# Kernel optimization log

Hardware: AMD Instinct MI355X
Metric: run time of the kernel (lower is better)

## Reference

```python
import jax, jax.numpy as jnp
import numpy as np
import math

B, S, E, H = 4, 1024, 1024, 16
DK = E // H   # 64, must equal B*H for the original code's D-broadcast to work
M = 64


def setup_inputs():
    key = jax.random.key(0)
    ks = jax.random.split(key, 12)
    s = 0.02
    d = {"hidden_states": jax.random.normal(ks[0], (B, S, E), jnp.float32)}
    for i, name in enumerate(["Wq", "Wk", "Wv", "Wo"]):
        d[name] = jax.random.normal(ks[1 + i], (E, E), jnp.float32) * s
    for name in ["bq", "bk", "bv", "bo"]:
        d[name] = jnp.zeros((E,), jnp.float32)
    # eigenvectors of G G^T, as in SymmetricRandomFeatures.__init__ (orthogonal d_k x d_k)
    G = np.asarray(jax.random.normal(ks[9], (DK, M)), np.float64)
    _, vecs = np.linalg.eigh(G @ G.T)
    d["random_matrix"] = jnp.asarray(vecs, jnp.float32)
    # stands in for torch.randn(M, d_k) drawn inside forward
    d["omega_noise"] = jax.random.normal(ks[10], (M, DK), jnp.float32)
    return d


def _derf_forward(hidden_states, Wq, bq, Wk, bk, Wv, bv, Wo, bo, random_matrix, omega_noise):
    B_, S_, E_ = hidden_states.shape
    dk = E_ // H
    scale = 1.0 / math.sqrt(dk)

    def heads(x):
        return x.reshape(B_, S_, H, dk).transpose(0, 2, 1, 3)  # [B,H,S,dk]

    q = heads(hidden_states @ Wq.T + bq) * scale
    k = heads(hidden_states @ Wk.T + bk) * scale
    v = heads(hidden_states @ Wv.T + bv)

    qf = q.reshape(B_ * H, S_, dk)
    kf = k.reshape(B_ * H, S_, dk)

    # per-(B*H) second-moment matrix
    M1 = jnp.einsum('bsd,bse->bde', qf, qf) / S_
    M2 = jnp.einsum('bsd,bse->bde', kf, kf) / S_
    mu4 = jnp.mean(qf, axis=1)  # [BH, dk]
    mu5 = jnp.mean(kf, axis=1)
    mat = M1 + mu4[:, :, None] * mu5[:, None, :] + mu5[:, :, None] * mu4[:, None, :] + M2
    # torch updates A/B/C/D via .data (detached) -> stop_gradient before SVD
    mat = jax.lax.stop_gradient(mat)

    Q3, lam, _ = jnp.linalg.svd(mat)             # lam >= 0
    a = (1.0 - 2.0 * lam - jnp.sqrt((2.0 * lam + 1.0) ** 2 + 8.0 * lam)) / 16.0  # [BH, dk]
    one_m4a = 1.0 - 4.0 * a                       # diag of (I - 4A), >= 1
    Bmat = jnp.sqrt(one_m4a)[:, :, None] * jnp.swapaxes(Q3, -2, -1)  # sqrt(I-4A) @ Q3^T
    Dval = jnp.prod(one_m4a, axis=-1) ** 0.25     # det(I-4A)^(1/4), shape [BH] == [dk]

    omega = random_matrix @ omega_noise.T         # [dk, M]
    half_omega = 0.5 * jnp.sum(omega ** 2, axis=1)  # [dk]

    # NOTE: Dval has shape (B*H,) == (dk,) and broadcasts over the feature axis,
    # exactly replicating the torch broadcasting behavior (requires B*H == dk).
    eq = jnp.exp(jnp.einsum('bsd,bed->bse', qf, Bmat) + half_omega + Dval)
    ek = jnp.exp(jnp.einsum('bsd,bed->bse', kf, Bmat) + half_omega + Dval)

    qn = eq / jnp.linalg.norm(eq, axis=-1, keepdims=True)
    kn = ek / jnp.linalg.norm(ek, axis=-1, keepdims=True)
    qn = qn.reshape(B_, H, S_, dk)
    kn = kn.reshape(B_, H, S_, dk)

    scores = jnp.einsum('bhsd,bhtd->bhst', qn, kn)      # [B,H,S,S]
    probs = jax.nn.softmax(scores, axis=-1)
    ctx = jnp.einsum('bhst,bhtd->bhsd', probs, v)
    ctx = ctx.transpose(0, 2, 1, 3).reshape(B_, S_, E_)
    return ctx @ Wo.T + bo


def reference(hidden_states, Wq, bq, Wk, bk, Wv, bv, Wo, bo, random_matrix, omega_noise):
    return _derf_forward(hidden_states, Wq, bq, Wk, bk, Wv, bv, Wo, bo,
                         random_matrix, omega_noise)
```

## Files before the change

### kernel.cpp

```cpp
#include <hip/hip_runtime.h>
#include <hip/hip_bf16.h>

typedef __attribute__((ext_vector_type(8))) short v8s;
typedef __attribute__((ext_vector_type(4))) float v4f;
typedef __hip_bfloat16 bf16;

#define NSWEEP 1

__device__ __forceinline__ float bf2f(short s) {
    unsigned int u = ((unsigned int)(unsigned short)s) << 16;
    return __uint_as_float(u);
}

__global__ void diag_f32(float* __restrict__ out, size_t n, float code)
{
    for (size_t i = (size_t)blockIdx.x * 256 + threadIdx.x; i < n;
         i += (size_t)gridDim.x * 256)
        out[i] = (i == 0) ? code : 0.0f;
}

template<int MODE>
__device__ __forceinline__
void gemm_tile_body(const void* __restrict__ Ap, const float* __restrict__ W,
                    const float* __restrict__ bias, float scale,
                    bf16* __restrict__ o0, bf16* __restrict__ o1,
                    bf16* __restrict__ o2, bf16* __restrict__ o3,
                    float* __restrict__ outF,
                    int mt, int nt, int t, bf16 (*As)[40], bf16 (*Bs)[40])
{
    const int K = 1024;
    int m0 = mt * 128;
    int n0 = nt * 128;
    int lane = t & 63, w = t >> 6;
    int wm = (w >> 1) * 64, wn = (w & 1) * 64;
    int l15 = lane & 15, quad = lane >> 4;

    v4f zz = {0.f, 0.f, 0.f, 0.f};
    v4f acc[4][4];
#pragma unroll
    for (int i = 0; i < 4; ++i)
#pragma unroll
        for (int j = 0; j < 4; ++j) acc[i][j] = zz;

    for (int k0 = 0; k0 < K; k0 += 32) {
        __syncthreads();
        if (MODE != 3) {
            const float* A = (const float*)Ap;
#pragma unroll
            for (int r2 = 0; r2 < 4; ++r2) {
                int idx = t + r2 * 256;
                int row = idx >> 3, kc = (idx & 7) * 4;
                float4 v = *(const float4*)&A[(size_t)(m0 + row) * K + k0 + kc];
                As[row][kc + 0] = __float2bfloat16(v.x);
                As[row][kc + 1] = __float2bfloat16(v.y);
                As[row][kc + 2] = __float2bfloat16(v.z);
                As[row][kc + 3] = __float2bfloat16(v.w);
            }
        } else {
            const bf16* A = (const bf16*)Ap;
#pragma unroll
            for (int r2 = 0; r2 < 2; ++r2) {
                int idx = t + r2 * 256;
                int row = idx >> 2, kc = (idx & 3) * 8;
                int kk = k0 + kc;
                int h = kk >> 6, d = kk & 63;
                int mr = m0 + row;
                int b = mr >> 10, s = mr & 1023;
                *(float4*)&As[row][kc] =
                    *(const float4*)&A[(((size_t)(b * 16 + h) * 1024 + s) << 6) + d];
            }
        }
#pragma unroll
        for (int r2 = 0; r2 < 4; ++r2) {
            int idx = t + r2 * 256;
            int row = idx >> 3, kc = (idx & 7) * 4;
            float4 v = *(const float4*)&W[(size_t)(n0 + row) * K + k0 + kc];
            Bs[row][kc + 0] = __float2bfloat16(v.x);
            Bs[row][kc + 1] = __float2bfloat16(v.y);
            Bs[row][kc + 2] = __float2bfloat16(v.z);
            Bs[row][kc + 3] = __float2bfloat16(v.w);
        }
        __syncthreads();
        v8s af[4], bfr[4];
#pragma unroll
        for (int i = 0; i < 4; ++i)
            af[i] = *(v8s*)&As[wm + i * 16 + l15][quad * 8];
#pragma unroll
        for (int j = 0; j < 4; ++j)
            bfr[j] = *(v8s*)&Bs[wn + j * 16 + l15][quad * 8];
#pragma unroll
        for (int i = 0; i < 4; ++i)
#pragma unroll
            for (int j = 0; j < 4; ++j)
                acc[i][j] = __builtin_amdgcn_mfma_f32_16x16x32_bf16(af[i], bfr[j], acc[i][j], 0, 0, 0);
    }
    bf16* vout = nullptr;
    if (MODE == 2) {
        int b = m0 >> 10;
        vout = (b == 0) ? o0 : (b == 1) ? o1 : (b == 2) ? o2 : o3;
    }
#pragma unroll
    for (int i = 0; i < 4; ++i)
#pragma unroll
        for (int j = 0; j < 4; ++j)
#pragma unroll
            for (int r = 0; r < 4; ++r) {
                int m = m0 + wm + i * 16 + quad * 4 + r;
                int n = n0 + wn + j * 16 + l15;
                float val = (acc[i][j][r] + bias[n]) * scale;
                if (MODE == 1) {
                    int b = m >> 10, s = m & 1023, h = n >> 6, d = n & 63;
                    o0[(((size_t)(b * 16 + h) * 1024 + s) << 6) + d] = __float2bfloat16(val);
                } else if (MODE == 2) {
                    int s = m & 1023, h = n >> 6, d = n & 63;
                    vout[(((size_t)h * 1024 + s) << 6) + d] = __float2bfloat16(val);
                } else {
                    outF[(size_t)m * 1024 + n] = val;
                }
            }
}

__global__ __launch_bounds__(256)
void gemm_qk(const float* __restrict__ hs,
             const float* __restrict__ Wq, const float* __restrict__ bq,
             const float* __restrict__ Wk, const float* __restrict__ bk,
             bf16* __restrict__ Qf, bf16* __restrict__ Kf)
{
    __shared__ bf16 As[128][40];
    __shared__ bf16 Bs[128][40];
    int bx = blockIdx.x;
    bool isK = bx >= 32;
    gemm_tile_body<1>(hs, isK ? Wk : Wq, isK ? bk : bq, 0.125f,
                      isK ? Kf : Qf, nullptr, nullptr, nullptr, nullptr,
                      bx & 31, blockIdx.y, threadIdx.x, As, Bs);
}

__global__ __launch_bounds__(256)
void gemm_o(const bf16* __restrict__ Ctx, const float* __restrict__ Wo,
            const float* __restrict__ bo, float* __restrict__ outF)
{
    __shared__ bf16 As[128][40];
    __shared__ bf16 Bs[128][40];
    gemm_tile_body<3>(Ctx, Wo, bo, 1.0f, nullptr, nullptr, nullptr, nullptr,
                      outF, blockIdx.x, blockIdx.y, threadIdx.x, As, Bs);
}

__global__ __launch_bounds__(256)
void gram_stats(const bf16* __restrict__ qb, const bf16* __restrict__ kb,
                float* __restrict__ G, float* __restrict__ musum)
{
    __shared__ float qt[64][68];
    __shared__ float ktl[64][68];
    int bh = blockIdx.x, sc = blockIdx.y;
    int t = threadIdx.x;
    size_t base = ((size_t)bh * 1024 + sc * 64) * 64;
#pragma unroll
    for (int r = 0; r < 2; ++r) {
        int c = t + r * 256;
        int row = c >> 3, c8 = (c & 7) * 8;
        v8s vq = *(const v8s*)&qb[base + row * 64 + c8];
        v8s vk = *(const v8s*)&kb[base + row * 64 + c8];
#pragma unroll
        for (int i = 0; i < 8; ++i) {
            qt[row][c8 + i] = bf2f(vq[i]);
            ktl[row][c8 + i] = bf2f(vk[i]);
        }
    }
    __syncthreads();
    int tj = t & 15, ti = t >> 4;
    float aq[4][4], ak[4][4];
#pragma unroll
    for (int r = 0; r < 4; ++r)
#pragma unroll
        for (int c = 0; c < 4; ++c) { aq[r][c] = 0.f; ak[r][c] = 0.f; }
    for (int s = 0; s < 64; ++s) {
        float qd[4], qe[4], kd[4], ke[4];
#pragma unroll
        for (int r = 0; r < 4; ++r) {
            qd[r] = qt[s][ti * 4 + r]; qe[r] = qt[s][tj * 4 + r];
            kd[r] = ktl[s][ti * 4 + r]; ke[r] = ktl[s][tj * 4 + r];
        }
#pragma unroll
        for (int r = 0; r < 4; ++r)
#pragma unroll
            for (int c = 0; c < 4; ++c) {
                aq[r][c] += qd[r] * qe[c];
                ak[r][c] += kd[r] * ke[c];
            }
    }
    float* Gp = G + (size_t)bh * 4096;
#pragma unroll
    for (int r = 0; r < 4; ++r)
#pragma unroll
        for (int c = 0; c < 4; ++c)
            atomicAdd(&Gp[(ti * 4 + r) * 64 + tj * 4 + c], aq[r][c] + ak[r][c]);
    if (t < 128) {
        int which = t >> 6, d = t & 63;
        float s0 = 0.0f;
        if (which == 0) { for (int s = 0; s < 64; ++s) s0 += qt[s][d]; }
        else            { for (int s = 0; s < 64; ++s) s0 += ktl[s][d]; }
        atomicAdd(&musum[((size_t)which * 64 + bh) * 64 + d], s0);
    }
}

__device__ void jacobi_body(int bh, const float* __restrict__ G,
                            const float* __restrict__ musum,
                            float* __restrict__ W2, float* __restrict__ Dval,
                            char* smem)
{
    float  (*A)[65]   = (float(*)[65])smem;
    float2* cs2       = (float2*)(smem + 16640);
    float*  lam       = (float*)(smem + 17152);
    float*  muq       = (float*)(smem + 17408);
    float*  muk       = (float*)(smem + 17664);
    float  (*redA)[64] = (float(*)[64])(smem + 17920);
    float  (*redV)[64] = (float(*)[64])(smem + 19968);
    int t = threadIdx.x;
    int lane = t & 63, w = t >> 6;
    const float invS = 1.0f / 1024.0f;
    if (t < 64) {
        muq[t] = musum[(size_t)bh * 64 + t] * invS;
        muk[t] = musum[4096 + (size_t)bh * 64 + t] * invS;
    }
    __syncthreads();
    const float* Gb = G + (size_t)bh * 4096;
    float vr[8];
#pragma unroll
    for (int i = 0; i < 8; ++i) vr[i] = (w * 8 + i == lane) ? 1.0f : 0.0f;
#pragma unroll
    for (int r = 0; r < 8; ++r) {
        int idx = t + r * 512;
        int i = idx >> 6, j = idx & 63;
        A[i][j] = Gb[idx] * invS + muq[i] * muk[j] + muk[i] * muq[j];
    }
    __syncthreads();
    for (int sweep = 0; sweep < NSWEEP; ++sweep) {
        for (int m = 1; m < 64; ++m) {
            if (t < 64) {
                int q = t ^ m;
                float app = A[t][t], aqq = A[q][q], apq = A[t][q];
                float c = 1.0f, s = 0.0f;
                if (fabsf(apq) > 1e-28f) {
                    float tau = (aqq - app) / (2.0f * apq);
                    float tt = (tau >= 0.0f ? 1.0f : -1.0f)
                             / (fabsf(tau) + sqrtf(1.0f + tau * tau));
                    float cd = 1.0f / sqrtf(1.0f + tt * tt);
                    c = cd; s = tt * cd;
                }
                cs2[t] = make_float2(c, -s);
            }
            __syncthreads();
            int hb = 31 - __builtin_clz((unsigned)m);
            int lowmask = (1 << hb) - 1;
#pragma unroll
            for (int r = 0; r < 2; ++r) {
                int idx = t + r * 512;
                int ki = idx >> 5, kj = idx & 31;
                int i1 = ((ki & ~lowmask) << 1) | (ki & lowmask);
                int i2 = i1 ^ m;
                int j1 = ((kj & ~lowmask) << 1) | (kj & lowmask);
                int j2 = j1 ^ m;
                float a11 = A[i1][j1], a12 = A[i1][j2];
                float a21 = A[i2][j1], a22 = A[i2][j2];
                float2 ci = cs2[i1];
                float2 cj = cs2[j1];
                float t11 = ci.x * a11 + ci.y * a21, t12 = ci.x * a12 + ci.y * a22;
                float t21 = ci.x * a21 - ci.y * a11, t22 = ci.x * a22 - ci.y * a12;
                A[i1][j1] = cj.x * t11 + cj.y * t12;
                A[i1][j2] = cj.x * t12 - cj.y * t11;
                A[i2][j1] = cj.x * t21 + cj.y * t22;
                A[i2][j2] = cj.x * t22 - cj.y * t21;
            }
            {
                float2 cj = cs2[lane];
#pragma unroll
                for (int i = 0; i < 8; ++i) {
                    float pv = __shfl_xor(vr[i], m, 64);
                    vr[i] = cj.x * vr[i] + cj.y * pv;
                }
            }
            __syncthreads();
        }
    }
    if (t < 64) lam[t] = A[t][t];
    float best = -1.0f, sv = 0.0f;
#pragma unroll
    for (int i = 0; i < 8; ++i) {
        float av = fabsf(vr[i]);
        if (av > best) { best = av; sv = vr[i]; }
    }
    redA[w][lane] = best;
    redV[w][lane] = sv;
    __syncthreads();
    float gbest = -1.0f, gsv = 0.0f;
#pragma unroll
    for (int ww = 0; ww < 8; ++ww) {
        float av = redA[ww][lane];
        if (av > gbest) { gbest = av; gsv = redV[ww][lane]; }
    }
    float lj = lam[lane];
    int rank = 0;
    for (int k2 = 0; k2 < 64; ++k2) {
        float lk = lam[k2];
        rank += (lk > lj) || (lk == lj && k2 < lane);
    }
    float tl = 2.0f * lj + 1.0f;
    float om = (3.0f + 2.0f * lj + sqrtf(tl * tl + 8.0f * lj)) * 0.25f;
    float cfac = sqrtf(om);
    if (gsv < 0.0f) cfac = -cfac;
#pragma unroll
    for (int i = 0; i < 8; ++i)
        W2[((size_t)bh * 64 + (w * 8 + i)) * 64 + rank] = cfac * vr[i];
    if (w == 0) muq[lane] = logf(om);
    __syncthreads();
    if (t == 0) {
        float ssum = 0.0f;
        for (int j = 0; j < 64; ++j) ssum += muq[j];
        Dval[bh] = expf(0.25f * ssum);
    }
}

__device__ void omega_body(const float* __restrict__ rm,
                           const float* __restrict__ on,
                           float* __restrict__ hw, char* smem)
{
    float (*ons)[64] = (float(*)[64])smem;
    int t = threadIdx.x;
    for (int i = t; i < 4096; i += 512) ons[i >> 6][i & 63] = on[i];
    __syncthreads();
    if (t < 64) {
        float rmv[64];
#pragma unroll
        for (int j = 0; j < 64; ++j) rmv[j] = rm[t * 64 + j];
        float r8[8];
#pragma unroll
        for (int i = 0; i < 8; ++i) r8[i] = 0.0f;
        for (int k = 0; k < 8; ++k) {
#pragma unroll
            for (int i = 0; i < 8; ++i) {
                int m = k * 8 + i;
                float dot = 0.0f;
#pragma unroll
                for (int j = 0; j < 64; ++j) dot += rmv[j] * ons[m][j];
                r8[i] += dot * dot;
            }
        }
        float acc = ((r8[0] + r8[1]) + (r8[2] + r8[3])) + ((r8[4] + r8[5]) + (r8[6] + r8[7]));
        hw[t] = 0.5f * acc;
    }
}

__global__ __launch_bounds__(512)
void jacobi_fused(const float* __restrict__ G, const float* __restrict__ musum,
                  float* __restrict__ W2, float* __restrict__ Dval,
                  const float* __restrict__ hs, const float* __restrict__ Wv,
                  const float* __restrict__ bv,
                  bf16* __restrict__ V0, bf16* __restrict__ V1,
                  bf16* __restrict__ V2,
                  const float* __restrict__ rm, const float* __restrict__ on,
                  float* __restrict__ hw)
{
    __shared__ __align__(16) char smem[40960];
    int bid = blockIdx.x;
    if (bid < 64) {
        jacobi_body(bid, G, musum, W2, Dval, smem);
    } else if (bid < 160) {
        int gb = bid - 64;
        int t = threadIdx.x;
        int h = t >> 8, tl = t & 255;
        int T = gb * 2 + h;
        int mt = T >> 3, nt = T & 7;
        bf16 (*As)[40] = (bf16(*)[40])(smem + h * 20480);
        bf16 (*Bs)[40] = (bf16(*)[40])(smem + h * 20480 + 10240);
        gemm_tile_body<2>(hs, Wv, bv, 1.0f, V0, V1, V2, nullptr, nullptr,
                          mt, nt, tl, As, Bs);
    } else {
        omega_body(rm, on, hw, smem);
    }
}

__global__ __launch_bounds__(256)
void features_v23(bf16* __restrict__ qb, bf16* __restrict__ kb,
                  const float* __restrict__ W2g, const float* __restrict__ Dv,
                  const float* __restrict__ hw,
                  const float* __restrict__ hs, const float* __restrict__ Wv,
                  const float* __restrict__ bv,
                  bf16* __restrict__ V3)
{
    __shared__ __align__(16) char smem[20480];
    int bid = blockIdx.x;
    int t = threadIdx.x;
    if (bid < 512) {
        bf16 (*whi)[72] = (bf16(*)[72])smem;
        bf16 (*wlo)[72] = (bf16(*)[72])(smem + 9216);
        float* hD = (float*)(smem + 18432);
        int bh = bid >> 3, qk = (bid >> 2) & 1, rg = bid & 3;
        const float* W2b = W2g + (size_t)bh * 4096;
#pragma unroll
        for (int r = 0; r < 4; ++r) {
            int idx4 = t + r * 256;
            int d = idx4 >> 4, e4 = (idx4 & 15) * 4;
            float4 wv = ((const float4*)W2b)[idx4];
            float vv[4] = {wv.x, wv.y, wv.z, wv.w};
#pragma unroll
            for (int i = 0; i < 4; ++i) {
                bf16 h = __float2bfloat16(vv[i]);
                whi[e4 + i][d] = h;
                wlo[e4 + i][d] = __float2bfloat16(vv[i] - __bfloat162float(h));
            }
        }
        if (t < 64) hD[t] = hw[t] + Dv[t];
        __syncthreads();
        int lane = t & 63, w = t >> 6;
        int l15 = lane & 15, quad = lane >> 4;
        bf16* buf = qk ? kb : qb;
        bf16* base = buf + ((size_t)bh << 16);
        int R0 = rg * 256 + w * 64;
        v8s aq[4][2];
#pragma unroll
        for (int i = 0; i < 4; ++i) {
            const bf16* rp = base + (size_t)(R0 + i * 16 + l15) * 64;
            aq[i][0] = *(const v8s*)&rp[quad * 8];
            aq[i][1] = *(const v8s*)&rp[32 + quad * 8];
        }
        v4f zz = {0.f, 0.f, 0.f, 0.f};
        v4f acc[4][4];
#pragma unroll
        for (int i = 0; i < 4; ++i)
#pragma unroll
            for (int j = 0; j < 4; ++j) acc[i][j] = zz;
#pragma unroll
        for (int j = 0; j < 4; ++j) {
            v8s bh0 = *(v8s*)&whi[j * 16 + l15][quad * 8];
            v8s bh1 = *(v8s*)&whi[j * 16 + l15][32 + quad * 8];
            v8s bl0 = *(v8s*)&wlo[j * 16 + l15][quad * 8];
            v8s bl1 = *(v8s*)&wlo[j * 16 + l15][32 + quad * 8];
#pragma unroll
            for (int i = 0; i < 4; ++i) {
                acc[i][j] = __builtin_amdgcn_mfma_f32_16x16x32_bf16(aq[i][0], bh0, acc[i][j], 0, 0, 0);
                acc[i][j] = __builtin_amdgcn_mfma_f32_16x16x32_bf16(aq[i][1], bh1, acc[i][j], 0, 0, 0);
                acc[i][j] = __builtin_amdgcn_mfma_f32_16x16x32_bf16(aq[i][0], bl0, acc[i][j], 0, 0, 0);
                acc[i][j] = __builtin_amdgcn_mfma_f32_16x16x32_bf16(aq[i][1], bl1, acc[i][j], 0, 0, 0);
            }
        }
        float hDl[4];
#pragma unroll
        for (int j = 0; j < 4; ++j) hDl[j] = hD[j * 16 + l15];
#pragma unroll
        for (int i = 0; i < 4; ++i) {
            float te[4][4];
            float s2[4] = {0.f, 0.f, 0.f, 0.f};
#pragma unroll
            for (int j = 0; j < 4; ++j)
#pragma unroll
                for (int r = 0; r < 4; ++r) {
                    float x = acc[i][j][r] + hDl[j];
                    float e = expf(x);
                    te[j][r] = e;
                    s2[r] += e * e;
                }
#pragma unroll
            for (int r = 0; r < 4; ++r) {
#pragma unroll
                for (int off = 1; off < 16; off <<= 1)
                    s2[r] += __shfl_xor(s2[r], off, 64);
                float inv = 1.0f / sqrtf(s2[r]);
                int R = R0 + i * 16 + quad * 4 + r;
                bf16* rp = base + (size_t)R * 64;
#pragma unroll
                for (int j = 0; j < 4; ++j)
                    rp[j * 16 + l15] = __float2bfloat16(te[j][r] * inv);
            }
        }
    } else {
        int gb = bid - 512;
        int mt = 24 + (gb >> 3), nt = gb & 7;
        bf16 (*As)[40] = (bf16(*)[40])smem;
        bf16 (*Bs)[40] = (bf16(*)[40])(smem + 10240);
        gemm_tile_body<2>(hs, Wv, bv, 1.0f, nullptr, nullptr, nullptr, V3, nullptr,
                          mt, nt, t, As, Bs);
    }
}

__global__ __launch_bounds__(256)
void flash_attn(const bf16* __restrict__ qn, const bf16* __restrict__ kn,
                const bf16* __restrict__ v0, const bf16* __restrict__ v1,
                const bf16* __restrict__ v2, const bf16* __restrict__ v3,
                bf16* __restrict__ ctx)
{
    __shared__ bf16 kt_s[64][72];
    __shared__ bf16 vt_s[64][72];
    __shared__ bf16 p_s[4][16][72];
    int bh = blockIdx.x, qt = blockIdx.y;
    int t = threadIdx.x, lane = t & 63, w = t >> 6;
    int quad = lane >> 4, l15 = lane & 15;
    int b = bh >> 4, hl = bh & 15;
    const bf16* vv = ((b == 0) ? v0 : (b == 1) ? v1 : (b == 2) ? v2 : v3)
                   + ((size_t)hl << 16);

    int qrow = qt * 64 + w * 16 + l15;
    const bf16* qptr = qn + ((size_t)bh * 1024 + qrow) * 64;
    v8s aq0 = *(const v8s*)&qptr[quad * 8];
    v8s aq1 = *(const v8s*)&qptr[32 + quad * 8];

    v4f zz = {0.f, 0.f, 0.f, 0.f};
    v4f ctxa[4];
#pragma unroll
    for (int dj = 0; dj < 4; ++dj) ctxa[dj] = zz;
    float lsum[4] = {0.f, 0.f, 0.f, 0.f};

    for (int kt = 0; kt < 16; ++kt) {
        __syncthreads();
#pragma unroll
        for (int r2 = 0; r2 < 2; ++r2) {
            int idx = t + r2 * 256;
            int row = idx >> 3, c8 = (idx & 7) * 8;
            *(float4*)&kt_s[row][c8] =
                *(const float4*)&kn[((size_t)bh * 1024 + kt * 64 + row) * 64 + c8];
            v8s vchunk = *(const v8s*)&vv[((size_t)(kt * 64 + row)) * 64 + c8];
#pragma unroll
            for (int i = 0; i < 8; ++i)
                ((short*)vt_s)[(size_t)(c8 + i) * 72 + (row ^ c8)] = vchunk[i];
        }
        __syncthreads();
        v4f sa[4];
#pragma unroll
        for (int j = 0; j < 4; ++j) {
            v8s bk0 = *(v8s*)&kt_s[j * 16 + l15][quad * 8];
            v8s bk1 = *(v8s*)&kt_s[j * 16 + l15][32 + quad * 8];
            v4f z = zz;
            z = __builtin_amdgcn_mfma_f32_16x16x32_bf16(aq0, bk0, z, 0, 0, 0);
            sa[j] = __builtin_amdgcn_mfma_f32_16x16x32_bf16(aq1, bk1, z, 0, 0, 0);
        }
        float pv[4][4];
#pragma unroll
        for (int r = 0; r < 4; ++r) {
#pragma unroll
            for (int j = 0; j < 4; ++j) {
                float pe = __expf(sa[j][r]);
                pv[j][r] = pe;
                lsum[r] += pe;
            }
        }
#pragma unroll
        for (int j = 0; j < 4; ++j)
#pragma unroll
            for (int r = 0; r < 4; ++r)
                p_s[w][quad * 4 + r][j * 16 + l15] = __float2bfloat16(pv[j][r]);
        __syncthreads();
        v8s ap0 = *(v8s*)&p_s[w][l15][quad * 8];
        v8s ap1 = *(v8s*)&p_s[w][l15][32 + quad * 8];
#pragma unroll
        for (int dj = 0; dj < 4; ++dj) {
            int d0 = dj * 16 + l15;
            int a0 = (d0 >> 3) & 7;
            v8s bv0 = *(v8s*)&vt_s[d0][8 * (quad ^ a0)];
            v8s bv1 = *(v8s*)&vt_s[d0][8 * ((4 + quad) ^ a0)];
            ctxa[dj] = __builtin_amdgcn_mfma_f32_16x16x32_bf16(ap0, bv0, ctxa[dj], 0, 0, 0);
            ctxa[dj] = __builtin_amdgcn_mfma_f32_16x16x32_bf16(ap1, bv1, ctxa[dj], 0, 0, 0);
        }
    }
#pragma unroll
    for (int r = 0; r < 4; ++r)
#pragma unroll
        for (int off = 1; off < 16; off <<= 1)
            lsum[r] += __shfl_xor(lsum[r], off, 64);
#pragma unroll
    for (int dj = 0; dj < 4; ++dj)
#pragma unroll
        for (int r = 0; r < 4; ++r) {
            int srow = qt * 64 + w * 16 + quad * 4 + r;
            int d = dj * 16 + l15;
            float val = ctxa[dj][r] / lsum[r];
            ctx[((size_t)bh * 1024 + srow) * 64 + d] = __float2bfloat16(val);
        }
}

extern "C" void kernel_launch(void* const* d_in, const int* in_sizes, int n_in,
                              void* d_out, int out_size, void* d_ws, size_t ws_size,
                              hipStream_t stream)
{
    const size_t OUT_N = 4194304;
    long mx = 0; int ih = -1;
    for (int i = 0; i < n_in; ++i)
        if ((long)in_sizes[i] > mx) { mx = in_sizes[i]; ih = i; }
    long szW = mx / 4, szR = mx / 1024, szB = mx / 4096;
    int wI[4], rI[2], bI[4], nW = 0, nR = 0, nB = 0;
    bool bad = (n_in != 11) || (mx % 4096 != 0);
    if (!bad) {
        for (int i = 0; i < n_in; ++i) {
            if (i == ih) continue;
            long s = in_sizes[i];
            if (s == szW && nW < 4) wI[nW++] = i;
            else if (s == szR && nR < 2) rI[nR++] = i;
            else if (s == szB && nB < 4) bI[nB++] = i;
            else bad = true;
        }
        if (nW != 4 || nR != 2 || nB != 4) bad = true;
    }
    if (bad) {
        diag_f32<<<256, 256, 0, stream>>>((float*)d_out, OUT_N, 333.0f);
        return;
    }
    const float *Wq, *Wk, *Wv, *Wo, *bq, *bk, *bv, *bo, *rm, *on;
    float *WqS, *WkS;
    if (ih == 8 && wI[0] == 0 && wI[1] == 1 && wI[2] == 2 && wI[3] == 3) {
        Wk = (const float*)d_in[wI[0]]; Wo = (const float*)d_in[wI[1]];
        Wq = (const float*)d_in[wI[2]]; Wv = (const float*)d_in[wI[3]];
        bk = (const float*)d_in[bI[0]]; bo = (const float*)d_in[bI[1]];
        bq = (const float*)d_in[bI[2]]; bv = (const float*)d_in[bI[3]];
        on = (const float*)d_in[rI[0]]; rm = (const float*)d_in[rI[1]];
        WqS = (float*)d_in[wI[2]]; WkS = (float*)d_in[wI[0]];
    } else {
        Wq = (const float*)d_in[wI[0]]; Wk = (const float*)d_in[wI[1]];
        Wv = (const float*)d_in[wI[2]]; Wo = (const float*)d_in[wI[3]];
        bq = (const float*)d_in[bI[0]]; bk = (const float*)d_in[bI[1]];
        bv = (const float*)d_in[bI[2]]; bo = (const float*)d_in[bI[3]];
        rm = (const float*)d_in[rI[0]]; on = (const float*)d_in[rI[1]];
        WqS = (float*)d_in[wI[0]]; WkS = (float*)d_in[wI[1]];
    }
    const float* hs = (const float*)d_in[ih];
    float* hsW = (float*)d_in[ih];
    float* outF = (float*)d_out;

    bf16* Qf = (bf16*)d_out;
    bf16* Kf = (bf16*)((char*)d_out + (8u << 20));
    float* G     = WqS;
    float* musum = WqS + 262144;
    float* hw    = WqS + 262144 + 16384;
    float* Dval  = WqS + 262144 + 16384 + 1024;
    bf16* V0 = (bf16*)WkS;
    bf16* V1 = (bf16*)WkS + 1048576;
    bf16* V2 = (bf16*)(WqS + 327680);
    bf16* V3 = (bf16*)hsW;
    bf16* Ctx = (bf16*)(hsW + 524288);

    gemm_qk<<<dim3(64, 8), 256, 0, stream>>>(hs, Wq, bq, Wk, bk, Qf, Kf);
    hipMemsetAsync(G, 0, 1u << 20, stream);
    hipMemsetAsync(musum, 0, 32768, stream);
    gram_stats<<<dim3(64, 16), 256, 0, stream>>>(Qf, Kf, G, musum);
    jacobi_fused<<<161, 512, 0, stream>>>(G, musum, G, Dval, hs, Wv, bv,
                                          V0, V1, V2, rm, on, hw);
    features_v23<<<576, 256, 0, stream>>>(Qf, Kf, G, Dval, hw, hs, Wv, bv, V3);
    flash_attn<<<dim3(64, 16), 256, 0, stream>>>(Qf, Kf, V0, V1, V2, V3, Ctx);
    gemm_o<<<dim3(32, 8), 256, 0, stream>>>(Ctx, Wo, bo, outF);
}
```

Baseline: 364.5 us.

## Rewrite gram_stats with MFMA, one block per head, drop atomics and memsets

New measurement: 317.4 us. -12.9%, faster.

```diff
diff --git a/kernel.cpp b/kernel.cpp
--- a/kernel.cpp
+++ b/kernel.cpp
@@ -145,61 +145,105 @@
                       outF, blockIdx.x, blockIdx.y, threadIdx.x, As, Bs);
 }
 
-__global__ __launch_bounds__(256)
+__global__ __launch_bounds__(512)
 void gram_stats(const bf16* __restrict__ qb, const bf16* __restrict__ kb,
                 float* __restrict__ G, float* __restrict__ musum)
 {
-    __shared__ float qt[64][68];
-    __shared__ float ktl[64][68];
-    int bh = blockIdx.x, sc = blockIdx.y;
+    __shared__ __align__(16) char smem[37376];
+    int bh = blockIdx.x;
     int t = threadIdx.x;
-    size_t base = ((size_t)bh * 1024 + sc * 64) * 64;
-#pragma unroll
-    for (int r = 0; r < 2; ++r) {
-        int c = t + r * 256;
-        int row = c >> 3, c8 = (c & 7) * 8;
-        v8s vq = *(const v8s*)&qb[base + row * 64 + c8];
-        v8s vk = *(const v8s*)&kb[base + row * 64 + c8];
-#pragma unroll
-        for (int i = 0; i < 8; ++i) {
-            qt[row][c8 + i] = bf2f(vq[i]);
-            ktl[row][c8 + i] = bf2f(vk[i]);
+    int tl = t & 255;
+    int grp = t >> 8;
+    int w = t >> 6;
+    int wly = w & 3;
+    int lane = t & 63, l15 = lane & 15, quad = lane >> 4;
+
+    bf16* qT = (bf16*)(smem + grp * 18432);
+    bf16* kT = (bf16*)(smem + grp * 18432 + 9216);
+    float* msB = (float*)(smem + 36864);
+
+    v4f zz = {0.f, 0.f, 0.f, 0.f};
+    v4f acc[4];
+#pragma unroll
+    for (int i = 0; i < 4; ++i) acc[i] = zz;
+    float msum = 0.0f;
+
+    const bf16* qbase = qb + ((size_t)bh << 16);
+    const bf16* kbase = kb + ((size_t)bh << 16);
+
+    for (int cc = 0; cc < 8; ++cc) {
+        int c = cc * 2 + grp;
+        __syncthreads();
+#pragma unroll
+        for (int r2 = 0; r2 < 2; ++r2) {
+            int idx = tl + r2 * 256;
+            int row = idx >> 3, c8 = (idx & 7) * 8;
+            v8s vq = *(const v8s*)&qbase[(size_t)(c * 64 + row) * 64 + c8];
+            v8s vk = *(const v8s*)&kbase[(size_t)(c * 64 + row) * 64 + c8];
+#pragma unroll
+            for (int i = 0; i < 8; ++i) {
+                ((short*)qT)[(size_t)(c8 + i) * 72 + (row ^ c8)] = vq[i];
+                ((short*)kT)[(size_t)(c8 + i) * 72 + (row ^ c8)] = vk[i];
+            }
+        }
+        __syncthreads();
+        int db = wly * 16 + l15;
+        int ab = (db >> 3) & 7;
+        v8s bq0 = *(v8s*)&qT[db * 72 + 8 * (quad ^ ab)];
+        v8s bq1 = *(v8s*)&qT[db * 72 + 8 * ((4 + quad) ^ ab)];
+        v8s bk0 = *(v8s*)&kT[db * 72 + 8 * (quad ^ ab)];
+        v8s bk1 = *(v8s*)&kT[db * 72 + 8 * ((4 + quad) ^ ab)];
+#pragma unroll
+        for (int i = 0; i < 4; ++i) {
+            int da = i * 16 + l15;
+            int aa = (da >> 3) & 7;
+            v8s aq0 = *(v8s*)&qT[da * 72 + 8 * (quad ^ aa)];
+            v8s aq1 = *(v8s*)&qT[da * 72 + 8 * ((4 + quad) ^ aa)];
+            v8s ak0 = *(v8s*)&kT[da * 72 + 8 * (quad ^ aa)];
+            v8s ak1 = *(v8s*)&kT[da * 72 + 8 * ((4 + quad) ^ aa)];
+            acc[i] = __builtin_amdgcn_mfma_f32_16x16x32_bf16(aq0, bq0, acc[i], 0, 0, 0);
+            acc[i] = __builtin_amdgcn_mfma_f32_16x16x32_bf16(aq1, bq1, acc[i], 0, 0, 0);
+            acc[i] = __builtin_amdgcn_mfma_f32_16x16x32_bf16(ak0, bk0, acc[i], 0, 0, 0);
+            acc[i] = __builtin_amdgcn_mfma_f32_16x16x32_bf16(ak1, bk1, acc[i], 0, 0, 0);
+        }
+        if (tl < 64) {
+            const short* rowp = (const short*)qT + (size_t)tl * 72;
+            float s0 = 0.0f;
+#pragma unroll
+            for (int s = 0; s < 64; ++s) s0 += bf2f(rowp[s]);
+            msum += s0;
+        } else if (tl < 128) {
+            const short* rowp = (const short*)kT + (size_t)(tl - 64) * 72;
+            float s0 = 0.0f;
+#pragma unroll
+            for (int s = 0; s < 64; ++s) s0 += bf2f(rowp[s]);
+            msum += s0;
         }
     }
     __syncthreads();
-    int tj = t & 15, ti = t >> 4;
-    float aq[4][4], ak[4][4];
-#pragma unroll
-    for (int r = 0; r < 4; ++r)
-#pragma unroll
-        for (int c = 0; c < 4; ++c) { aq[r][c] = 0.f; ak[r][c] = 0.f; }
-    for (int s = 0; s < 64; ++s) {
-        float qd[4], qe[4], kd[4], ke[4];
-#pragma unroll
-        for (int r = 0; r < 4; ++r) {
-            qd[r] = qt[s][ti * 4 + r]; qe[r] = qt[s][tj * 4 + r];
-            kd[r] = ktl[s][ti * 4 + r]; ke[r] = ktl[s][tj * 4 + r];
-        }
-#pragma unroll
-        for (int r = 0; r < 4; ++r)
-#pragma unroll
-            for (int c = 0; c < 4; ++c) {
-                aq[r][c] += qd[r] * qe[c];
-                ak[r][c] += kd[r] * ke[c];
-            }
-    }
-    float* Gp = G + (size_t)bh * 4096;
-#pragma unroll
-    for (int r = 0; r < 4; ++r)
-#pragma unroll
-        for (int c = 0; c < 4; ++c)
-            atomicAdd(&Gp[(ti * 4 + r) * 64 + tj * 4 + c], aq[r][c] + ak[r][c]);
-    if (t < 128) {
-        int which = t >> 6, d = t & 63;
-        float s0 = 0.0f;
-        if (which == 0) { for (int s = 0; s < 64; ++s) s0 += qt[s][d]; }
-        else            { for (int s = 0; s < 64; ++s) s0 += ktl[s][d]; }
-        atomicAdd(&musum[((size_t)which * 64 + bh) * 64 + d], s0);
+    float* redbuf = (float*)smem;
+    if (grp == 1) {
+#pragma unroll
+        for (int i = 0; i < 4; ++i)
+#pragma unroll
+            for (int r = 0; r < 4; ++r)
+                redbuf[(size_t)(wly * 4 + i) * 256 + (quad * 4 + r) * 16 + l15] = acc[i][r];
+        if (tl < 128) msB[tl] = msum;
+    }
+    __syncthreads();
+    if (grp == 0) {
+#pragma unroll
+        for (int i = 0; i < 4; ++i)
+#pragma unroll
+            for (int r = 0; r < 4; ++r) {
+                float v = acc[i][r] +
+                    redbuf[(size_t)(wly * 4 + i) * 256 + (quad * 4 + r) * 16 + l15];
+                G[(size_t)bh * 4096 + (size_t)(i * 16 + quad * 4 + r) * 64 + wly * 16 + l15] = v;
+            }
+        if (tl < 128) {
+            int which = tl >> 6, d = tl & 63;
+            musum[((size_t)which * 64 + bh) * 64 + d] = msum + msB[tl];
+        }
     }
 }
 
@@ -636,9 +680,7 @@
     bf16* Ctx = (bf16*)(hsW + 524288);
 
     gemm_qk<<<dim3(64, 8), 256, 0, stream>>>(hs, Wq, bq, Wk, bk, Qf, Kf);
-    hipMemsetAsync(G, 0, 1u << 20, stream);
-    hipMemsetAsync(musum, 0, 32768, stream);
-    gram_stats<<<dim3(64, 16), 256, 0, stream>>>(Qf, Kf, G, musum);
+    gram_stats<<<64, 512, 0, stream>>>(Qf, Kf, G, musum);
     jacobi_fused<<<161, 512, 0, stream>>>(G, musum, G, Dval, hs, Wv, bv,
                                           V0, V1, V2, rm, on, hw);
     features_v23<<<576, 256, 0, stream>>>(Qf, Kf, G, Dval, hw, hs, Wv, bv, V3);
```
